# Kernel tuning notes

Hardware: AMD Instinct MI355X
Metric: run time of the kernel (lower is better)

## Reference

```python
import jax, jax.numpy as jnp
import numpy as np

H = 16
D_MODEL = 1024
D_K = D_MODEL // H
B, S = 2, 2048


def setup_inputs() -> dict:
    key = jax.random.key(0)
    ks = jax.random.split(key, 11)
    scale = 1.0 / np.sqrt(D_MODEL)
    inp = {
        "query": jax.random.normal(ks[0], (B, S, D_MODEL), jnp.float32),
        "key": jax.random.normal(ks[1], (B, S, D_MODEL), jnp.float32),
        "value": jax.random.normal(ks[2], (B, S, D_MODEL), jnp.float32),
        # four nn.Linear(d_model, d_model): Wq, Wk, Wv, Wo (torch convention: y = x @ W.T + b)
        "Wq": jax.random.uniform(ks[3], (D_MODEL, D_MODEL), jnp.float32, -scale, scale),
        "bq": jax.random.uniform(ks[4], (D_MODEL,), jnp.float32, -scale, scale),
        "Wk": jax.random.uniform(ks[5], (D_MODEL, D_MODEL), jnp.float32, -scale, scale),
        "bk": jax.random.uniform(ks[6], (D_MODEL,), jnp.float32, -scale, scale),
        "Wv": jax.random.uniform(ks[7], (D_MODEL, D_MODEL), jnp.float32, -scale, scale),
        "bv": jax.random.uniform(ks[8], (D_MODEL,), jnp.float32, -scale, scale),
        "Wo": jax.random.uniform(ks[9], (D_MODEL, D_MODEL), jnp.float32, -scale, scale),
        "bo": jax.random.uniform(ks[10], (D_MODEL,), jnp.float32, -scale, scale),
    }
    return inp


def _split_heads(x):
    # [B, S, D] -> [B, H, S, d_k]
    b, s, _ = x.shape
    return x.reshape(b, s, H, D_K).transpose(0, 2, 1, 3)


def reference(query, key, value, Wq, bq, Wk, bk, Wv, bv, Wo, bo):
    q = _split_heads(query @ Wq.T + bq)
    k = _split_heads(key @ Wk.T + bk)
    v = _split_heads(value @ Wv.T + bv)
    # scaled dot-product attention (dropout omitted: reference is eval-mode)
    scores = jnp.einsum("bhqd,bhkd->bhqk", q, k) / np.sqrt(D_K).astype(np.float32)
    p = jax.nn.softmax(scores, axis=-1)
    x = jnp.einsum("bhqk,bhkd->bhqd", p, v)
    x = x.transpose(0, 2, 1, 3).reshape(query.shape[0], -1, H * D_K)
    return x @ Wo.T + bo
```

## Files before the change

### kernel.cpp

```cpp
#include <hip/hip_runtime.h>

typedef unsigned short u16;
typedef unsigned int u32;
typedef __attribute__((ext_vector_type(8))) short short8;
typedef __attribute__((ext_vector_type(4))) float floatx4;
typedef __attribute__((ext_vector_type(4))) unsigned short ushortx4;
typedef __attribute__((ext_vector_type(2))) unsigned int uint2v;

#define DEV static __device__ __forceinline__

DEV float bf2f(u16 u) { union { unsigned u; float f; } v; v.u = ((unsigned)u) << 16; return v.f; }
DEV u16 f2bf(float f) {
  union { float f; unsigned u; } v; v.f = f;
  return (u16)((v.u + 0x7FFFu + ((v.u >> 16) & 1u)) >> 16);
}
DEV u32 pkbf(float a, float b) {
  union { float f; u32 u; } x, y; x.f = a; y.f = b;
  return __builtin_amdgcn_perm(y.u + 0x8000u, x.u + 0x8000u, 0x07060302u);
}
DEV float fexp2(float x) { return __builtin_amdgcn_exp2f(x); }

#define GLDS(g, l) __builtin_amdgcn_global_load_lds( \
    (const __attribute__((address_space(1))) void*)(g), \
    (__attribute__((address_space(3))) void*)(l), 16, 0, 0)

struct CvtArg {
  const float* src[11];
  u16* dst[11];
  int cum[12];
};

__global__ void convert(CvtArg a) {
  const long base = ((long)blockIdx.x * 256 + threadIdx.x) * 4;
  if (base >= a.cum[11]) return;
  int s = 0;
  while (s < 10 && base >= a.cum[s + 1]) ++s;
  const long off = base - a.cum[s];
  const float* sp = a.src[s] + off;
  ushortx4 u;
#pragma unroll
  for (int r = 0; r < 4; ++r) u[r] = f2bf(sp[r]);
  *(ushortx4*)(a.dst[s] + off) = u;
}

struct GemmArg {
  const u16* x;
  const u16* w;
  const u16* bias;
  u16* dst;
  int mode;
};

__global__ __launch_bounds__(256, 2) void gemm_nt(GemmArg g0, GemmArg g1, GemmArg g2) {
  GemmArg g = (blockIdx.z == 0) ? g0 : ((blockIdx.z == 1) ? g1 : g2);
  __shared__ u16 As[128 * 32];
  __shared__ u16 Bs[128 * 32];
  const int tid = threadIdx.x, w = tid >> 6, l = tid & 63;
  const int l15 = l & 15, quad = l >> 4;
  const int bm = blockIdx.x, bn = blockIdx.y;
  const int wm = w >> 1, wn = w & 1;

  floatx4 acc[4][4];
#pragma unroll
  for (int i = 0; i < 4; ++i)
#pragma unroll
    for (int j = 0; j < 4; ++j) acc[i][j] = (floatx4){0.f, 0.f, 0.f, 0.f};

  const u16* xb = g.x + (long)(bm * 128 + w * 16 + (l >> 2)) * 1024 + (l & 3) * 8;
  const u16* wb = g.w + (long)(bn * 128 + w * 16 + (l >> 2)) * 1024 + (l & 3) * 8;
  u16* asb = &As[(w * 16) * 32];
  u16* bsb = &Bs[(w * 16) * 32];

  for (int kt = 0; kt < 32; ++kt) {
    const int k0 = kt * 32;
    __syncthreads();
#pragma unroll
    for (int p = 0; p < 2; ++p) {
      GLDS(xb + (long)p * 64 * 1024 + k0, asb + p * 64 * 32);
      GLDS(wb + (long)p * 64 * 1024 + k0, bsb + p * 64 * 32);
    }
    __syncthreads();
    short8 af[4], bfr[4];
#pragma unroll
    for (int mi = 0; mi < 4; ++mi)
      af[mi] = *(const short8*)&As[(wm * 64 + mi * 16 + l15) * 32 + quad * 8];
#pragma unroll
    for (int ni = 0; ni < 4; ++ni)
      bfr[ni] = *(const short8*)&Bs[(wn * 64 + ni * 16 + l15) * 32 + quad * 8];
#pragma unroll
    for (int mi = 0; mi < 4; ++mi)
#pragma unroll
      for (int ni = 0; ni < 4; ++ni)
        acc[mi][ni] = __builtin_amdgcn_mfma_f32_16x16x32_bf16(af[mi], bfr[ni], acc[mi][ni], 0, 0, 0);
  }

  float bv[4];
#pragma unroll
  for (int ni = 0; ni < 4; ++ni) bv[ni] = bf2f(g.bias[bn * 128 + wn * 64 + ni * 16 + l15]);

#pragma unroll
  for (int mi = 0; mi < 4; ++mi) {
    const int mbase = bm * 128 + wm * 64 + mi * 16 + quad * 4;
#pragma unroll
    for (int ni = 0; ni < 4; ++ni) {
      const int n = bn * 128 + wn * 64 + ni * 16 + l15;
      if (g.mode == 2) {
        const int b = mbase >> 11, s = mbase & 2047;
        const int h = n >> 6, d = n & 63;
        ushortx4 u;
#pragma unroll
        for (int r = 0; r < 4; ++r) u[r] = f2bf(acc[mi][ni][r] + bv[ni]);
        *(ushortx4*)&g.dst[((long)(b * 16 + h) * 64 + d) * 2048 + s] = u;
      } else if (g.mode == 3) {
        float* df = (float*)g.dst;
#pragma unroll
        for (int r = 0; r < 4; ++r)
          df[(long)(mbase + r) * 1024 + n] = acc[mi][ni][r] + bv[ni];
      } else {
        const float sc = (g.mode == 0) ? 0.18033688011f : 1.0f;
        const int h = n >> 6, d = n & 63;
#pragma unroll
        for (int r = 0; r < 4; ++r) {
          const int m = mbase + r, b = m >> 11, s = m & 2047;
          g.dst[((long)(b * 16 + h) * 2048 + s) * 64 + d] = f2bf((acc[mi][ni][r] + bv[ni]) * sc);
        }
      }
    }
  }
}

__global__ __launch_bounds__(256, 2) void attn_flash(const u16* __restrict__ Q,
                                                     const u16* __restrict__ K,
                                                     const u16* __restrict__ V,
                                                     u16* __restrict__ X) {
  __shared__ u16 Ks[2][64 * 72];
  __shared__ u16 Vs[2][64 * 72];
  __shared__ u16 Ps[4][32 * 72];
  __shared__ float denW[4][32];
  const int tid = threadIdx.x, w = tid >> 6, l = tid & 63;
  const int l15 = l & 15, quad = l >> 4;
  const int q0 = blockIdx.x * 128, bh = blockIdx.y;
  const u16* qp = Q + (long)bh * 2048 * 64;
  const u16* kp = K + (long)bh * 2048 * 64;
  const u16* vp = V + (long)bh * 2048 * 64;

  const int r0 = tid >> 3, c0 = tid & 7;
  const int r1 = (256 + tid) >> 3, c1 = tid & 7;

#define ISSUE_LOADS(kv0) \
    sk0 = *(const short8*)(kp + (long)((kv0) + r0) * 64 + c0 * 8); \
    sv0 = *(const short8*)(vp + (long)r0 * 2048 + (kv0) + c0 * 8); \
    sk1 = *(const short8*)(kp + (long)((kv0) + r1) * 64 + c1 * 8); \
    sv1 = *(const short8*)(vp + (long)r1 * 2048 + (kv0) + c1 * 8);

#define STORE_TILE(pb) \
    *(short8*)&Ks[pb][r0 * 72 + c0 * 8] = sk0; \
    *(short8*)&Vs[pb][r0 * 72 + c0 * 8] = sv0; \
    *(short8*)&Ks[pb][r1 * 72 + c1 * 8] = sk1; \
    *(short8*)&Vs[pb][r1 * 72 + c1 * 8] = sv1;

  short8 sk0, sv0, sk1, sv1;

  short8 qf[2][2];
#pragma unroll
  for (int nq = 0; nq < 2; ++nq)
#pragma unroll
    for (int kc = 0; kc < 2; ++kc)
      qf[nq][kc] = *(const short8*)(qp + (long)(q0 + w * 32 + nq * 16 + l15) * 64 + kc * 32 + quad * 8);

  floatx4 o[2][4];
#pragma unroll
  for (int mq = 0; mq < 2; ++mq)
#pragma unroll
    for (int nd = 0; nd < 4; ++nd) o[mq][nd] = (floatx4){0.f, 0.f, 0.f, 0.f};
  float den[2] = {0.f, 0.f};

  ISSUE_LOADS(0)
  STORE_TILE(0)
  ISSUE_LOADS(64)
  __syncthreads();

  for (int t = 0; t < 32; ++t) {
    const int p = t & 1;

#pragma unroll
    for (int mk = 0; mk < 4; ++mk) {
      short8 ak0 = *(const short8*)&Ks[p][(mk * 16 + l15) * 72 + quad * 8];
      short8 ak1 = *(const short8*)&Ks[p][(mk * 16 + l15) * 72 + 32 + quad * 8];
#pragma unroll
      for (int nq = 0; nq < 2; ++nq) {
        floatx4 st = (floatx4){0.f, 0.f, 0.f, 0.f};
        st = __builtin_amdgcn_mfma_f32_16x16x32_bf16(ak0, qf[nq][0], st, 0, 0, 0);
        st = __builtin_amdgcn_mfma_f32_16x16x32_bf16(ak1, qf[nq][1], st, 0, 0, 0);
        const float e0 = fexp2(st[0]), e1 = fexp2(st[1]);
        const float e2 = fexp2(st[2]), e3 = fexp2(st[3]);
        den[nq] += (e0 + e1) + (e2 + e3);
        uint2v pk = { pkbf(e0, e1), pkbf(e2, e3) };
        *(uint2v*)&Ps[w][(nq * 16 + l15) * 72 + mk * 16 + quad * 4] = pk;
      }
    }

#pragma unroll
    for (int kc = 0; kc < 2; ++kc) {
      short8 ap0 = *(const short8*)&Ps[w][l15 * 72 + kc * 32 + quad * 8];
      short8 ap1 = *(const short8*)&Ps[w][(16 + l15) * 72 + kc * 32 + quad * 8];
#pragma unroll
      for (int nd = 0; nd < 4; ++nd) {
        short8 bvf = *(const short8*)&Vs[p][(nd * 16 + l15) * 72 + kc * 32 + quad * 8];
        o[0][nd] = __builtin_amdgcn_mfma_f32_16x16x32_bf16(ap0, bvf, o[0][nd], 0, 0, 0);
        o[1][nd] = __builtin_amdgcn_mfma_f32_16x16x32_bf16(ap1, bvf, o[1][nd], 0, 0, 0);
      }
    }

    if (t < 31) {
      STORE_TILE(p ^ 1)
      if (t < 30) {
        const int nxt = (t + 2) * 64;
        ISSUE_LOADS(nxt)
      }
    }
    __syncthreads();
  }

#pragma unroll
  for (int nq = 0; nq < 2; ++nq) {
    float d = den[nq];
    d += __shfl_xor(d, 16);
    d += __shfl_xor(d, 32);
    if (l < 16) denW[w][nq * 16 + l] = 1.0f / d;
  }

  const int b = bh >> 4, h = bh & 15;
#pragma unroll
  for (int mq = 0; mq < 2; ++mq) {
#pragma unroll
    for (int r = 0; r < 4; ++r) {
      const float rcp = denW[w][mq * 16 + quad * 4 + r];
      const int s = q0 + w * 32 + mq * 16 + quad * 4 + r;
      u16* xrow = X + ((long)(b * 2048 + s)) * 1024 + h * 64;
#pragma unroll
      for (int nd = 0; nd < 4; ++nd)
        xrow[nd * 16 + l15] = f2bf(o[mq][nd][r] * rcp);
    }
  }
}

extern "C" void kernel_launch(void* const* d_in, const int* in_sizes, int n_in,
                              void* d_out, int out_size, void* d_ws, size_t ws_size,
                              hipStream_t stream) {
  u16* ws = (u16*)d_ws;
  const size_t M1 = 1048576, M4 = 4194304;
  u16* NQ  = ws;
  u16* NK  = ws + M4;
  u16* NV  = ws + 2 * M4;
  u16* NWQ = ws + 3 * M4;
  u16* NWK = ws + 3 * M4 + M1;
  u16* NWV = ws + 3 * M4 + 2 * M1;
  u16* NWO = ws + 3 * M4 + 3 * M1;
  u16* NBQ = ws + 3 * M4 + 4 * M1;
  u16* NBK = NBQ + 1024;
  u16* NBV = NBQ + 2048;
  u16* NBO = NBQ + 3072;
  u16* Qb = ws + 16 * M1 + 8192;
  u16* Kb = Qb + M4;
  u16* Vb = Qb + 2 * M4;
  u16* Xb = NQ;

  CvtArg ca;
  u16* dsts[11] = {NQ, NK, NV, NWQ, NBQ, NWK, NBK, NWV, NBV, NWO, NBO};
  int sizes[11] = {(int)M4, (int)M4, (int)M4, (int)M1, 1024, (int)M1, 1024, (int)M1, 1024, (int)M1, 1024};
  int c = 0;
  for (int i = 0; i < 11; ++i) {
    ca.src[i] = (const float*)d_in[i];
    ca.dst[i] = dsts[i];
    ca.cum[i] = c;
    c += sizes[i];
  }
  ca.cum[11] = c;
  convert<<<(c / 4 + 255) / 256, 256, 0, stream>>>(ca);

  GemmArg gq{NQ, NWQ, NBQ, Qb, 0};
  GemmArg gk{NK, NWK, NBK, Kb, 1};
  GemmArg gv{NV, NWV, NBV, Vb, 2};
  gemm_nt<<<dim3(32, 8, 3), 256, 0, stream>>>(gq, gk, gv);

  attn_flash<<<dim3(16, 32), 256, 0, stream>>>(Qb, Kb, Vb, Xb);

  GemmArg go{Xb, NWO, NBO, (u16*)d_out, 3};
  gemm_nt<<<dim3(32, 8, 1), 256, 0, stream>>>(go, go, go);
}
```

Baseline: 227.6 us.

## Keep softmax probabilities in registers via lane shuffles, read V directly from global

The attention kernel no longer stages P through shared memory. The exponentiated scores are packed in registers and rearranged with an xor-shuffle butterfly, and the PV product is recast as V^T·P^T so that layout fits the MFMA operand. V fragments are loaded straight from global memory instead of being double-buffered in LDS, and the output is written as 4-wide vector stores. The grid is flattened and remapped so blocks sharing a batch-head land on the same XCD for L2 reuse. This cuts LDS traffic and footprint but adds shuffle instructions and uncached global V loads in the inner loop.

```diff
diff --git a/kernel.cpp b/kernel.cpp
--- a/kernel.cpp
+++ b/kernel.cpp
@@ -5,7 +5,7 @@
 typedef __attribute__((ext_vector_type(8))) short short8;
 typedef __attribute__((ext_vector_type(4))) float floatx4;
 typedef __attribute__((ext_vector_type(4))) unsigned short ushortx4;
-typedef __attribute__((ext_vector_type(2))) unsigned int uint2v;
+typedef __attribute__((ext_vector_type(4))) unsigned int uint4v;
 
 #define DEV static __device__ __forceinline__
 
@@ -134,32 +134,29 @@
                                                      const u16* __restrict__ V,
                                                      u16* __restrict__ X) {
   __shared__ u16 Ks[2][64 * 72];
-  __shared__ u16 Vs[2][64 * 72];
-  __shared__ u16 Ps[4][32 * 72];
-  __shared__ float denW[4][32];
   const int tid = threadIdx.x, w = tid >> 6, l = tid & 63;
   const int l15 = l & 15, quad = l >> 4;
-  const int q0 = blockIdx.x * 128, bh = blockIdx.y;
+
+  const int bid = blockIdx.x;
+  const int xcd = bid & 7, idx = bid >> 3;
+  const int qx = idx & 15, bh = xcd + 8 * (idx >> 4);
+  const int q0 = qx * 128;
+
   const u16* qp = Q + (long)bh * 2048 * 64;
   const u16* kp = K + (long)bh * 2048 * 64;
   const u16* vp = V + (long)bh * 2048 * 64;
 
-  const int r0 = tid >> 3, c0 = tid & 7;
-  const int r1 = (256 + tid) >> 3, c1 = tid & 7;
-
-#define ISSUE_LOADS(kv0) \
+  const int r0 = tid >> 3, c0 = tid & 7, r1 = 32 + (tid >> 3);
+
+#define ISSUE_K(kv0) \
     sk0 = *(const short8*)(kp + (long)((kv0) + r0) * 64 + c0 * 8); \
-    sv0 = *(const short8*)(vp + (long)r0 * 2048 + (kv0) + c0 * 8); \
-    sk1 = *(const short8*)(kp + (long)((kv0) + r1) * 64 + c1 * 8); \
-    sv1 = *(const short8*)(vp + (long)r1 * 2048 + (kv0) + c1 * 8);
-
-#define STORE_TILE(pb) \
-    *(short8*)&Ks[pb][r0 * 72 + c0 * 8] = sk0; \
-    *(short8*)&Vs[pb][r0 * 72 + c0 * 8] = sv0; \
-    *(short8*)&Ks[pb][r1 * 72 + c1 * 8] = sk1; \
-    *(short8*)&Vs[pb][r1 * 72 + c1 * 8] = sv1;
-
-  short8 sk0, sv0, sk1, sv1;
+    sk1 = *(const short8*)(kp + (long)((kv0) + r1) * 64 + c0 * 8);
+
+#define STORE_K(pb_) \
+    *(short8*)&Ks[pb_][r0 * 72 + c0 * 8] = sk0; \
+    *(short8*)&Ks[pb_][r1 * 72 + c0 * 8] = sk1;
+
+  short8 sk0, sk1;
 
   short8 qf[2][2];
 #pragma unroll
@@ -170,19 +167,42 @@
 
   floatx4 o[2][4];
 #pragma unroll
-  for (int mq = 0; mq < 2; ++mq)
-#pragma unroll
-    for (int nd = 0; nd < 4; ++nd) o[mq][nd] = (floatx4){0.f, 0.f, 0.f, 0.f};
+  for (int nq = 0; nq < 2; ++nq)
+#pragma unroll
+    for (int nd = 0; nd < 4; ++nd) o[nq][nd] = (floatx4){0.f, 0.f, 0.f, 0.f};
   float den[2] = {0.f, 0.f};
 
-  ISSUE_LOADS(0)
-  STORE_TILE(0)
-  ISSUE_LOADS(64)
+  const bool p1 = (l & 32) != 0;
+  const bool p3 = (l & 16) != 0;
+  const bool p2 = p1 ^ p3;
+
+#define BFLY(pbv, m00, m01, m10, m11) { \
+    u32 A0 = p1 ? (m10) : (m00), A1 = p1 ? (m11) : (m01); \
+    u32 s0_ = p1 ? (m00) : (m10), s1_ = p1 ? (m01) : (m11); \
+    u32 B0 = (u32)__shfl_xor((int)s0_, 32), B1 = (u32)__shfl_xor((int)s1_, 32); \
+    u32 t0 = p2 ? A0 : B0, t1 = p2 ? A1 : B1; \
+    u32 u0 = (u32)__shfl_xor((int)t0, 16), u1 = (u32)__shfl_xor((int)t1, 16); \
+    u32 w0 = p2 ? B0 : A0, w1 = p2 ? B1 : A1; \
+    pbv[0] = p3 ? u0 : w0; pbv[1] = p3 ? u1 : w1; \
+    pbv[2] = p3 ? w0 : u0; pbv[3] = p3 ? w1 : u1; \
+  }
+
+  ISSUE_K(0)
+  STORE_K(0)
+  ISSUE_K(64)
   __syncthreads();
 
   for (int t = 0; t < 32; ++t) {
     const int p = t & 1;
 
+    short8 vf[2][4];
+#pragma unroll
+    for (int kc = 0; kc < 2; ++kc)
+#pragma unroll
+      for (int nd = 0; nd < 4; ++nd)
+        vf[kc][nd] = *(const short8*)(vp + (long)(nd * 16 + l15) * 2048 + (long)t * 64 + kc * 32 + quad * 8);
+
+    u32 pk[2][4][2];
 #pragma unroll
     for (int mk = 0; mk < 4; ++mk) {
       short8 ak0 = *(const short8*)&Ks[p][(mk * 16 + l15) * 72 + quad * 8];
@@ -195,52 +215,53 @@
         const float e0 = fexp2(st[0]), e1 = fexp2(st[1]);
         const float e2 = fexp2(st[2]), e3 = fexp2(st[3]);
         den[nq] += (e0 + e1) + (e2 + e3);
-        uint2v pk = { pkbf(e0, e1), pkbf(e2, e3) };
-        *(uint2v*)&Ps[w][(nq * 16 + l15) * 72 + mk * 16 + quad * 4] = pk;
+        pk[nq][mk][0] = pkbf(e0, e1);
+        pk[nq][mk][1] = pkbf(e2, e3);
       }
     }
 
 #pragma unroll
     for (int kc = 0; kc < 2; ++kc) {
-      short8 ap0 = *(const short8*)&Ps[w][l15 * 72 + kc * 32 + quad * 8];
-      short8 ap1 = *(const short8*)&Ps[w][(16 + l15) * 72 + kc * 32 + quad * 8];
-#pragma unroll
-      for (int nd = 0; nd < 4; ++nd) {
-        short8 bvf = *(const short8*)&Vs[p][(nd * 16 + l15) * 72 + kc * 32 + quad * 8];
-        o[0][nd] = __builtin_amdgcn_mfma_f32_16x16x32_bf16(ap0, bvf, o[0][nd], 0, 0, 0);
-        o[1][nd] = __builtin_amdgcn_mfma_f32_16x16x32_bf16(ap1, bvf, o[1][nd], 0, 0, 0);
+#pragma unroll
+      for (int nq = 0; nq < 2; ++nq) {
+        uint4v pb;
+        BFLY(pb, pk[nq][2 * kc][0], pk[nq][2 * kc][1], pk[nq][2 * kc + 1][0], pk[nq][2 * kc + 1][1])
+        short8 pbs = __builtin_bit_cast(short8, pb);
+#pragma unroll
+        for (int nd = 0; nd < 4; ++nd)
+          o[nq][nd] = __builtin_amdgcn_mfma_f32_16x16x32_bf16(vf[kc][nd], pbs, o[nq][nd], 0, 0, 0);
       }
     }
 
     if (t < 31) {
-      STORE_TILE(p ^ 1)
+      STORE_K(p ^ 1)
       if (t < 30) {
-        const int nxt = (t + 2) * 64;
-        ISSUE_LOADS(nxt)
+        ISSUE_K((t + 2) * 64)
       }
     }
     __syncthreads();
   }
 
+  float rcp[2];
 #pragma unroll
   for (int nq = 0; nq < 2; ++nq) {
     float d = den[nq];
     d += __shfl_xor(d, 16);
     d += __shfl_xor(d, 32);
-    if (l < 16) denW[w][nq * 16 + l] = 1.0f / d;
+    rcp[nq] = 1.0f / d;
   }
 
   const int b = bh >> 4, h = bh & 15;
 #pragma unroll
-  for (int mq = 0; mq < 2; ++mq) {
-#pragma unroll
-    for (int r = 0; r < 4; ++r) {
-      const float rcp = denW[w][mq * 16 + quad * 4 + r];
-      const int s = q0 + w * 32 + mq * 16 + quad * 4 + r;
-      u16* xrow = X + ((long)(b * 2048 + s)) * 1024 + h * 64;
-#pragma unroll
-      for (int nd = 0; nd < 4; ++nd)
-        xrow[nd * 16 + l15] = f2bf(o[mq][nd][r] * rcp);
+  for (int nq = 0; nq < 2; ++nq) {
+    const int s = q0 + w * 32 + nq * 16 + l15;
+    u16* xrow = X + ((long)(b * 2048 + s)) * 1024 + h * 64;
+#pragma unroll
+    for (int nd = 0; nd < 4; ++nd) {
+      ushortx4 u;
+#pragma unroll
+      for (int r = 0; r < 4; ++r) u[r] = f2bf(o[nq][nd][r] * rcp[nq]);
+      *(ushortx4*)&xrow[nd * 16 + quad * 4] = u;
     }
   }
 }
@@ -284,7 +305,7 @@
   GemmArg gv{NV, NWV, NBV, Vb, 2};
   gemm_nt<<<dim3(32, 8, 3), 256, 0, stream>>>(gq, gk, gv);
 
-  attn_flash<<<dim3(16, 32), 256, 0, stream>>>(Qb, Kb, Vb, Xb);
+  attn_flash<<<dim3(512), 256, 0, stream>>>(Qb, Kb, Vb, Xb);
 
   GemmArg go{Xb, NWO, NBO, (u16*)d_out, 3};
   gemm_nt<<<dim3(32, 8, 1), 256, 0, stream>>>(go, go, go);
```

After: 244.3 us. 1.07x slower.
